# Optimization experiments

Hardware: AMD Instinct MI355X
Metric: run time of the kernel (lower is better)

## Reference

```python
import jax, jax.numpy as jnp
import numpy as np

B, T, C = 8, 2048, 1024
H = 4 * C
N_LAYER, LAYER_ID = 12, 2
K_CLAMP = 60.0
LN_EPS = 1e-5


def _ln(x, g, b):
    m = jnp.mean(x, axis=-1, keepdims=True)
    v = jnp.var(x, axis=-1, keepdims=True)
    return (x - m) * jax.lax.rsqrt(v + LN_EPS) * g + b


def _mix(x, time_mix, combined_mix):
    # x: (B,T,C). Causal shift (zeros at t=0), anti-causal shift (zeros at t=T-1).
    c = x.shape[-1]
    xm1 = jnp.pad(x[:, :-1], ((0, 0), (1, 0), (0, 0)))
    xp1 = jnp.pad(x[:, 1:], ((0, 0), (0, 1), (0, 0)))
    xc = jnp.concatenate([xm1[..., :c // 2], xp1[..., c // 2:]], axis=-1)
    return x * time_mix + xm1 * (1.0 - time_mix) + xc * combined_mix


def _wkv(time_decay, time_first, k, v):
    # RWKV WKV exponential-decay linear recurrence (the custom CUDA kernel).
    # k, v: (B,T,C); k > 0 (already clamped+exp'd).
    # y_t = (a_t + exp(u)*k_t*v_t) / (b_t + exp(u)*k_t)
    # a_{t+1} = exp(-exp(w))*a_t + k_t*v_t ; b likewise with v=1.
    ed = jnp.exp(-jnp.exp(time_decay))  # per-step channel decay, (C,)
    eu = jnp.exp(time_first)            # current-token bonus, (C,)

    def step(carry, kv_t):
        a, b = carry
        kt, vt = kv_t
        y = (a + eu * kt * vt) / (b + eu * kt)
        return (ed * a + kt * vt, ed * b + kt), y

    kT = jnp.swapaxes(k, 0, 1)  # (T,B,C)
    vT = jnp.swapaxes(v, 0, 1)
    z = jnp.zeros_like(kT[0])
    _, y = jax.lax.scan(step, (z, z), (kT, vT))
    return jnp.swapaxes(y, 0, 1)  # (B,T,C)


def _time_mix_block(x, time_mix, combined_mix, time_decay, time_first, Wk, Wv, Wr, Wo):
    xm = _mix(x, time_mix, combined_mix)
    k = jnp.exp(jnp.minimum(xm @ Wk.T, K_CLAMP))
    v = xm @ Wv.T
    r = xm @ Wr.T
    wkv = _wkv(time_decay, time_first, k, v)
    return (jax.nn.sigmoid(r) * wkv) @ Wo.T


def _channel_mix_block(x, time_mix, combined_mix, Fk, Fv, Fr):
    xm = _mix(x, time_mix, combined_mix)
    k = jnp.square(jax.nn.relu(xm @ Fk.T))
    kv = k @ Fv.T
    return jax.nn.sigmoid(xm @ Fr.T) * kv


def setup_inputs():
    key = jax.random.key(0)
    ks = jax.random.split(key, 9)
    s = 0.02
    x = jax.random.normal(ks[0], (B, T, C), jnp.float32)
    # time_decay init per the module (f1/f2 interpolation over layers)
    h = np.arange(C, dtype=np.float64)
    frac = (LAYER_ID - 1) / (N_LAYER - 2)
    f1 = 3.0 + frac * (1.2 - 3.0)
    f2 = 0.65 + frac * (0.4 - 0.65)
    decay_speed = np.power(f2, h / (C - 1) * 7.0) * f1
    tm = jnp.concatenate([jnp.zeros(C // 2), jnp.ones(C // 2)]).reshape(1, 1, C).astype(jnp.float32)
    return dict(
        x=x,
        ln1_g=jnp.ones((C,), jnp.float32), ln1_b=jnp.zeros((C,), jnp.float32),
        ln2_g=jnp.ones((C,), jnp.float32), ln2_b=jnp.zeros((C,), jnp.float32),
        att_time_mix=tm,
        att_combined_mix=jnp.full((1, 1, C), 0.01, jnp.float32),
        time_decay=jnp.asarray(np.log(decay_speed), jnp.float32),
        time_first=jnp.full((C,), float(np.log(0.3)), jnp.float32),
        Wk=jax.random.normal(ks[1], (C, C), jnp.float32) * s,
        Wv=jax.random.normal(ks[2], (C, C), jnp.float32) * s,
        Wr=jax.random.normal(ks[3], (C, C), jnp.float32) * s,
        Wo=jax.random.normal(ks[4], (C, C), jnp.float32) * s,
        ffn_time_mix=tm,
        ffn_combined_mix=jnp.full((1, 1, C), 0.01, jnp.float32),
        Fk=jax.random.normal(ks[5], (H, C), jnp.float32) * s,
        Fv=jax.random.normal(ks[6], (C, H), jnp.float32) * s,
        Fr=jax.random.normal(ks[7], (C, C), jnp.float32) * s,
    )


def reference(x, ln1_g, ln1_b, ln2_g, ln2_b, att_time_mix, att_combined_mix,
              time_decay, time_first, Wk, Wv, Wr, Wo,
              ffn_time_mix, ffn_combined_mix, Fk, Fv, Fr):
    x = _ln(x, ln1_g, ln1_b)
    x = x + _time_mix_block(x, att_time_mix, att_combined_mix, time_decay, time_first, Wk, Wv, Wr, Wo)
    x = _ln(x, ln2_g, ln2_b)
    x = x + _channel_mix_block(x, ffn_time_mix, ffn_combined_mix, Fk, Fv, Fr)
    return x
```

## Files before the change

### kernel.cpp

```cpp
#include <hip/hip_runtime.h>
#include <hip/hip_bf16.h>

typedef float f32x4 __attribute__((ext_vector_type(4)));
typedef __bf16 bf16x8 __attribute__((ext_vector_type(8)));
typedef __bf16 bf16x4 __attribute__((ext_vector_type(4)));

#define DEVI static __device__ __forceinline__

DEVI void glds16(const void* g, void* l) {
  __builtin_amdgcn_global_load_lds((__attribute__((address_space(1))) void*)g,
                                   (__attribute__((address_space(3))) void*)l, 16, 0, 0);
}

DEVI f32x4 load4(const float* p) { return *(const f32x4*)p; }
DEVI f32x4 load4(const __bf16* p) {
  bf16x4 v = *(const bf16x4*)p;
  f32x4 o = { (float)v[0], (float)v[1], (float)v[2], (float)v[3] };
  return o;
}
DEVI void store4(float* p, f32x4 v) { *(f32x4*)p = v; }
DEVI void store4(__bf16* p, f32x4 v) {
  bf16x4 o = { (__bf16)v[0], (__bf16)v[1], (__bf16)v[2], (__bf16)v[3] };
  *(bf16x4*)p = o;
}

__global__ void cvt_bf16(const float* __restrict__ in, __bf16* __restrict__ out, int n4) {
  int i = blockIdx.x * 256 + threadIdx.x;
  if (i < n4) {
    f32x4 v = *(const f32x4*)(in + (size_t)i * 4);
    store4(out + (size_t)i * 4, v);
  }
}

template <typename TIN, typename TOUT>
__global__ __launch_bounds__(256) void ln_kernel(const TIN* __restrict__ x,
    const float* __restrict__ gw, const float* __restrict__ bw,
    TOUT* __restrict__ out) {
  const size_t row = blockIdx.x;
  f32x4 v = load4(x + row * 1024 + threadIdx.x * 4);
  float s = v[0] + v[1] + v[2] + v[3];
  float q = v[0]*v[0] + v[1]*v[1] + v[2]*v[2] + v[3]*v[3];
#pragma unroll
  for (int o = 32; o > 0; o >>= 1) { s += __shfl_down(s, o); q += __shfl_down(q, o); }
  __shared__ float ss[4], qq[4];
  const int w = threadIdx.x >> 6, l = threadIdx.x & 63;
  if (l == 0) { ss[w] = s; qq[w] = q; }
  __syncthreads();
  s = ss[0] + ss[1] + ss[2] + ss[3];
  q = qq[0] + qq[1] + qq[2] + qq[3];
  const float mean = s * (1.0f / 1024.0f);
  const float var = q * (1.0f / 1024.0f) - mean * mean;
  const float rstd = rsqrtf(var + 1e-5f);
  f32x4 g4 = *(const f32x4*)(gw + threadIdx.x * 4);
  f32x4 b4 = *(const f32x4*)(bw + threadIdx.x * 4);
  f32x4 o;
#pragma unroll
  for (int j = 0; j < 4; ++j) o[j] = (v[j] - mean) * rstd * g4[j] + b4[j];
  store4(out + row * 1024 + threadIdx.x * 4, o);
}

template <typename TIN>
__global__ __launch_bounds__(256) void mix_kernel(const TIN* __restrict__ x,
    const float* __restrict__ tm, const float* __restrict__ cm,
    __bf16* __restrict__ out) {
  const int idx = blockIdx.x * 256 + threadIdx.x;
  const int t = (idx >> 8) & 2047;
  const int c = (idx & 255) * 4;
  const size_t base = ((size_t)(idx >> 8) << 10) + c;
  f32x4 xv = load4(x + base);
  f32x4 xm1 = {0.f, 0.f, 0.f, 0.f}, xp1 = {0.f, 0.f, 0.f, 0.f};
  if (t > 0)    xm1 = load4(x + base - 1024);
  if (t < 2047) xp1 = load4(x + base + 1024);
  f32x4 tm4 = *(const f32x4*)(tm + c);
  f32x4 cm4 = *(const f32x4*)(cm + c);
  f32x4 xc = (c < 512) ? xm1 : xp1;
  f32x4 o;
#pragma unroll
  for (int j = 0; j < 4; ++j)
    o[j] = xv[j] * tm4[j] + xm1[j] * (1.0f - tm4[j]) + xc[j] * cm4[j];
  store4(out + base, o);
}

__global__ __launch_bounds__(256) void wkv_part(const __bf16* __restrict__ k,
    const __bf16* __restrict__ v, const float* __restrict__ td,
    float* __restrict__ scA, float* __restrict__ scB) {
  const int gid = blockIdx.x * 256 + threadIdx.x;
  const int c = gid & 1023;
  const int j = (gid >> 10) & 31;
  const int b = gid >> 15;
  const float ed = expf(-expf(td[c]));
  float A = 0.f, Bv = 0.f;
  size_t off = ((size_t)(b * 2048 + j * 64) << 10) + c;
#pragma unroll 4
  for (int i = 0; i < 64; ++i, off += 1024) {
    const float kt = (float)k[off];
    const float kv = kt * (float)v[off];
    A = ed * A + kv;
    Bv = ed * Bv + kt;
  }
  scA[gid] = A;
  scB[gid] = Bv;
}

__global__ __launch_bounds__(256) void wkv_scan(const float* __restrict__ td,
    float* __restrict__ scA, float* __restrict__ scB) {
  const int gid = blockIdx.x * 256 + threadIdx.x;
  const int c = gid & 1023;
  const int b = gid >> 10;
  const float edL = expf(-expf(td[c]) * 64.0f);
  float a = 0.f, bb = 0.f;
  size_t off = ((size_t)b << 15) + c;
  for (int j = 0; j < 32; ++j, off += 1024) {
    const float Aj = scA[off], Bj = scB[off];
    scA[off] = a;
    scB[off] = bb;
    a = edL * a + Aj;
    bb = edL * bb + Bj;
  }
}

__global__ __launch_bounds__(256) void wkv_apply(const __bf16* __restrict__ k,
    const __bf16* __restrict__ v, const __bf16* __restrict__ sr,
    const float* __restrict__ td, const float* __restrict__ tf,
    const float* __restrict__ scA, const float* __restrict__ scB,
    __bf16* __restrict__ srw) {
  const int gid = blockIdx.x * 256 + threadIdx.x;
  const int c = gid & 1023;
  const int j = (gid >> 10) & 31;
  const int b = gid >> 15;
  const float ed = expf(-expf(td[c]));
  const float eu = expf(tf[c]);
  float a = scA[gid], bb = scB[gid];
  size_t off = ((size_t)(b * 2048 + j * 64) << 10) + c;
#pragma unroll 4
  for (int i = 0; i < 64; ++i, off += 1024) {
    const float kt = (float)k[off];
    const float vt = (float)v[off];
    const float kv = kt * vt;
    const float y = (a + eu * kv) / (bb + eu * kt);
    srw[off] = (__bf16)((float)sr[off] * y);
    a = ed * a + kv;
    bb = ed * bb + kt;
  }
}

enum { EPI_NONE = 0, EPI_EXP, EPI_SIG, EPI_RELU2, EPI_RESID, EPI_FINAL, EPI_KVR };

#define SCHED0() __builtin_amdgcn_sched_barrier(0)
#define SBAR() { __builtin_amdgcn_s_barrier(); SCHED0(); }
#define VMW0() { asm volatile("s_waitcnt vmcnt(0)" ::: "memory"); SCHED0(); }
#define LGKM(n) { asm volatile("s_waitcnt lgkmcnt(" #n ")" ::: "memory"); SCHED0(); }

template <int EPI>
__global__ __launch_bounds__(256, 2) void gemm128(
    const __bf16* __restrict__ A, const __bf16* __restrict__ W,
    void* outp, const void* res, const void* sig, const int N, const int K) {
  __shared__ __bf16 sA[2][8192];
  __shared__ __bf16 sB[2][8192];
  const int tid = threadIdx.x;
  const int w = tid >> 6, l = tid & 63;
  const int wr = (w >> 1) << 6, wc = (w & 1) << 6;

  const int nwg = gridDim.x * gridDim.y;
  int wg = blockIdx.y * gridDim.x + blockIdx.x;
  wg = (wg & 7) * (nwg >> 3) + (wg >> 3);
  const int m0 = (wg / gridDim.x) << 7;
  const int n0 = (wg % gridDim.x) << 7;

  const int lr = l >> 3;
  const int lc = (l & 7) ^ lr;
  const size_t gA = (size_t)(m0 + w * 32 + lr) * K + lc * 8;
  const size_t gB = (size_t)(n0 + w * 32 + lr) * K + lc * 8;
  const int ldsD = w * 2048;

  const int NTK = K >> 6;

#define STG_A(buf, kt, g) glds16(A + gA + (size_t)(g) * 8 * K + (size_t)(kt) * 64, &sA[buf][ldsD + (g) * 512])
#define STG_B(buf, kt, g) glds16(W + gB + (size_t)(g) * 8 * K + (size_t)(kt) * 64, &sB[buf][ldsD + (g) * 512])

  const int rA = (wr + (l & 15)) * 64;
  const int rB = (wc + (l & 15)) * 64;
  const int csw = l & 7;
  const int k0 = l >> 4;
#define LDA(buf, mi, kk) (*(const bf16x8*)&sA[buf][rA + (mi) * 1024 + ((((kk) * 4 + k0) ^ csw) << 3)])
#define LDB(buf, ni, kk) (*(const bf16x8*)&sB[buf][rB + (ni) * 1024 + ((((kk) * 4 + k0) ^ csw) << 3)])

  f32x4 acc[4][4] = {};

#pragma unroll
  for (int g = 0; g < 4; ++g) STG_A(0, 0, g);
#pragma unroll
  for (int g = 0; g < 4; ++g) STG_B(0, 0, g);

  for (int kt = 0; kt < NTK; ++kt) {
    const int buf = kt & 1, nb = buf ^ 1;
    const bool st = (kt + 1 < NTK);
    VMW0();
    SBAR();
    if (st) {
#pragma unroll
      for (int g = 0; g < 4; ++g) STG_A(nb, kt + 1, g);
#pragma unroll
      for (int g = 0; g < 4; ++g) STG_B(nb, kt + 1, g);
    }
    SCHED0();
    bf16x8 a0[4], a1[4], b0[4], b1[4];
#pragma unroll
    for (int i = 0; i < 4; ++i) a0[i] = LDA(buf, i, 0);
#pragma unroll
    for (int i = 0; i < 4; ++i) b0[i] = LDB(buf, i, 0);
    SCHED0();
#pragma unroll
    for (int i = 0; i < 4; ++i) a1[i] = LDA(buf, i, 1);
#pragma unroll
    for (int i = 0; i < 4; ++i) b1[i] = LDB(buf, i, 1);
    SCHED0();
    LGKM(8);
    __builtin_amdgcn_s_setprio(1);
#pragma unroll
    for (int mi = 0; mi < 4; ++mi)
#pragma unroll
      for (int ni = 0; ni < 4; ++ni)
        acc[mi][ni] = __builtin_amdgcn_mfma_f32_16x16x32_bf16(a0[mi], b0[ni], acc[mi][ni], 0, 0, 0);
    __builtin_amdgcn_s_setprio(0); SCHED0();
    LGKM(0);
    __builtin_amdgcn_s_setprio(1);
#pragma unroll
    for (int mi = 0; mi < 4; ++mi)
#pragma unroll
      for (int ni = 0; ni < 4; ++ni)
        acc[mi][ni] = __builtin_amdgcn_mfma_f32_16x16x32_bf16(a1[mi], b1[ni], acc[mi][ni], 0, 0, 0);
    __builtin_amdgcn_s_setprio(0);
  }

  const int rl = (l >> 4) << 2, cl = l & 15;
#pragma unroll
  for (int mi = 0; mi < 4; ++mi) {
#pragma unroll
    for (int ni = 0; ni < 4; ++ni) {
#pragma unroll
      for (int e = 0; e < 4; ++e) {
        const int r = m0 + wr + mi * 16 + rl + e;
        const int cidx = n0 + wc + ni * 16 + cl;
        const size_t idx = (size_t)r * N + cidx;
        const float vacc = acc[mi][ni][e];
        if constexpr (EPI == EPI_NONE) {
          ((__bf16*)outp)[idx] = (__bf16)vacc;
        } else if constexpr (EPI == EPI_EXP) {
          ((__bf16*)outp)[idx] = (__bf16)expf(fminf(vacc, 60.0f));
        } else if constexpr (EPI == EPI_SIG) {
          ((__bf16*)outp)[idx] = (__bf16)(1.0f / (1.0f + expf(-vacc)));
        } else if constexpr (EPI == EPI_RELU2) {
          const float rv = fmaxf(vacc, 0.0f);
          ((__bf16*)outp)[idx] = (__bf16)(rv * rv);
        } else if constexpr (EPI == EPI_RESID) {
          ((__bf16*)outp)[idx] = (__bf16)(vacc + (float)((const __bf16*)res)[idx]);
        } else if constexpr (EPI == EPI_FINAL) {
          ((float*)outp)[idx] = ((const float*)res)[idx] + (float)((const __bf16*)sig)[idx] * vacc;
        } else {
          const int sel = cidx >> 10;
          const size_t oidx = (size_t)r * 1024 + (cidx & 1023);
          if (sel == 0)      ((__bf16*)outp)[oidx] = (__bf16)expf(fminf(vacc, 60.0f));
          else if (sel == 1) ((__bf16*)const_cast<void*>(res))[oidx] = (__bf16)vacc;
          else               ((__bf16*)const_cast<void*>(sig))[oidx] = (__bf16)(1.0f / (1.0f + expf(-vacc)));
        }
      }
    }
  }
}

extern "C" void kernel_launch(void* const* d_in, const int* in_sizes, int n_in,
                              void* d_out, int out_size, void* d_ws, size_t ws_size,
                              hipStream_t stream) {
  (void)in_sizes; (void)n_in; (void)out_size;
  const float* x    = (const float*)d_in[0];
  const float* ln1g = (const float*)d_in[1];
  const float* ln1b = (const float*)d_in[2];
  const float* ln2g = (const float*)d_in[3];
  const float* ln2b = (const float*)d_in[4];
  const float* atm  = (const float*)d_in[5];
  const float* acm  = (const float*)d_in[6];
  const float* td   = (const float*)d_in[7];
  const float* tf   = (const float*)d_in[8];
  const float* Wk   = (const float*)d_in[9];
  const float* Wv   = (const float*)d_in[10];
  const float* Wr   = (const float*)d_in[11];
  const float* Wo   = (const float*)d_in[12];
  const float* ftm  = (const float*)d_in[13];
  const float* fcm  = (const float*)d_in[14];
  const float* Fk   = (const float*)d_in[15];
  const float* Fv   = (const float*)d_in[16];
  const float* Fr   = (const float*)d_in[17];

  constexpr size_t C = 1024, T = 2048, Bs = 8, H = 4096;
  constexpr size_t NT = Bs * T;
  constexpr size_t NTC = NT * C;
  constexpr size_t CC = C * C;
  constexpr size_t CH = C * H;

  char* p = (char*)d_ws;
  auto takeb = [&](size_t elems) { __bf16* q = (__bf16*)p; p += elems * 2; return q; };
  __bf16* wKVR = takeb(3 * CC);
  __bf16* wWo  = takeb(CC);
  __bf16* wFk  = takeb(CH);
  __bf16* wFv  = takeb(CH);
  __bf16* wFr  = takeb(CC);
  __bf16* Ab   = takeb(NTC);
  __bf16* Bb   = takeb(NTC);
  __bf16* Db   = takeb(NTC);
  float* scA = (float*)p; p += Bs * 32 * C * 4;
  float* scB = (float*)p; p += Bs * 32 * C * 4;
  __bf16* kk = (__bf16*)p;
  const size_t used = (size_t)(p - (char*)d_ws);
  const size_t kkcap = ws_size > used ? ws_size - used : 0;
  int chunks = 4;
  if (kkcap >= NT * H * 2)          chunks = 1;
  else if (kkcap >= NT * H)         chunks = 2;
  __bf16* Cb = kk;
  __bf16* sr  = (__bf16*)d_out;
  float*  x3  = (float*)d_out;

  auto cvt = [&](const float* src, size_t n, __bf16* dst) {
    const int n4 = (int)(n / 4);
    cvt_bf16<<<dim3((n4 + 255) / 256), dim3(256), 0, stream>>>(src, dst, n4);
  };
  cvt(Wk, CC, wKVR); cvt(Wv, CC, wKVR + CC); cvt(Wr, CC, wKVR + 2 * CC);
  cvt(Wo, CC, wWo); cvt(Fk, CH, wFk); cvt(Fv, CH, wFv); cvt(Fr, CC, wFr);

  const dim3 blk(256);

  ln_kernel<float, __bf16><<<dim3((unsigned)NT), blk, 0, stream>>>(x, ln1g, ln1b, Ab);
  mix_kernel<__bf16><<<dim3((unsigned)(NTC / 1024)), blk, 0, stream>>>(Ab, atm, acm, Bb);
  gemm128<EPI_KVR><<<dim3(24, 128), blk, 0, stream>>>(Bb, wKVR, Cb, Db, sr, 3072, 1024);
  wkv_part<<<dim3(1024), blk, 0, stream>>>(Cb, Db, td, scA, scB);
  wkv_scan<<<dim3(32), blk, 0, stream>>>(td, scA, scB);
  wkv_apply<<<dim3(1024), blk, 0, stream>>>(Cb, Db, sr, td, tf, scA, scB, Bb);
  gemm128<EPI_RESID><<<dim3(8, 128), blk, 0, stream>>>(Bb, wWo, Ab, Ab, nullptr, 1024, 1024);
  ln_kernel<__bf16, float><<<dim3((unsigned)NT), blk, 0, stream>>>(Ab, ln2g, ln2b, x3);
  mix_kernel<float><<<dim3((unsigned)(NTC / 1024)), blk, 0, stream>>>(x3, ftm, fcm, Db);
  gemm128<EPI_SIG><<<dim3(8, 128), blk, 0, stream>>>(Db, wFr, Bb, nullptr, nullptr, 1024, 1024);
  const size_t Mc = NT / chunks;
  for (int ch = 0; ch < chunks; ++ch) {
    const size_t ro = (size_t)ch * Mc;
    gemm128<EPI_RELU2><<<dim3(32, (unsigned)(Mc / 128)), blk, 0, stream>>>(
        Db + ro * C, wFk, kk, nullptr, nullptr, 4096, 1024);
    gemm128<EPI_FINAL><<<dim3(8, (unsigned)(Mc / 128)), blk, 0, stream>>>(
        kk, wFv, (float*)d_out + ro * C, (const float*)d_out + ro * C,
        Bb + ro * C, 1024, 4096);
  }
}
```

Measured before the change: 798.3 us.

## Vectorize WKV kernels, merge weight conversion, simplify GEMM to single-buffered LDS

The three WKV kernels now handle four channels per thread with vector bf16/f32 loads and use a quarter of the blocks. The seven weight-conversion launches become one kernel writing into a contiguous workspace. The GEMM drops LDS double buffering, the explicit waitcnt/sched barriers, setprio and the occupancy hint, and uses plain __syncthreads around each K-tile load. That GEMM change removes the overlap of global-to-LDS copies with MFMA work, so the dominant GEMMs are likely to lose throughput, while the WKV and launch changes save only a little.

```diff
diff --git a/kernel.cpp b/kernel.cpp
--- a/kernel.cpp
+++ b/kernel.cpp
@@ -24,12 +24,28 @@
   *(bf16x4*)p = o;
 }
 
-__global__ void cvt_bf16(const float* __restrict__ in, __bf16* __restrict__ out, int n4) {
-  int i = blockIdx.x * 256 + threadIdx.x;
-  if (i < n4) {
-    f32x4 v = *(const f32x4*)(in + (size_t)i * 4);
-    store4(out + (size_t)i * 4, v);
-  }
+constexpr size_t C = 1024, T = 2048, Bs = 8, H = 4096;
+constexpr size_t NT = Bs * T;
+constexpr size_t NTC = NT * C;
+constexpr size_t CC = C * C;
+constexpr size_t CH = C * H;
+
+__global__ __launch_bounds__(256) void cvt_all(
+    const float* __restrict__ Wk, const float* __restrict__ Wv,
+    const float* __restrict__ Wr, const float* __restrict__ Wo,
+    const float* __restrict__ Fk, const float* __restrict__ Fv,
+    const float* __restrict__ Fr, __bf16* __restrict__ out) {
+  const size_t e = ((size_t)blockIdx.x * 256 + threadIdx.x) * 4;
+  const float* src; size_t rel;
+  if      (e < CC)          { src = Wk; rel = e; }
+  else if (e < 2 * CC)      { src = Wv; rel = e - CC; }
+  else if (e < 3 * CC)      { src = Wr; rel = e - 2 * CC; }
+  else if (e < 4 * CC)      { src = Wo; rel = e - 3 * CC; }
+  else if (e < 4 * CC + CH) { src = Fk; rel = e - 4 * CC; }
+  else if (e < 4 * CC + 2 * CH) { src = Fv; rel = e - 4 * CC - CH; }
+  else                      { src = Fr; rel = e - 4 * CC - 2 * CH; }
+  f32x4 v = *(const f32x4*)(src + rel);
+  store4(out + e, v);
 }
 
 template <typename TIN, typename TOUT>
@@ -85,37 +101,51 @@
     const __bf16* __restrict__ v, const float* __restrict__ td,
     float* __restrict__ scA, float* __restrict__ scB) {
   const int gid = blockIdx.x * 256 + threadIdx.x;
-  const int c = gid & 1023;
-  const int j = (gid >> 10) & 31;
-  const int b = gid >> 15;
-  const float ed = expf(-expf(td[c]));
-  float A = 0.f, Bv = 0.f;
+  const int c = (gid & 255) * 4;
+  const int j = (gid >> 8) & 31;
+  const int b = gid >> 13;
+  float ed[4], A[4] = {}, Bv[4] = {};
+#pragma unroll
+  for (int q = 0; q < 4; ++q) ed[q] = expf(-expf(td[c + q]));
   size_t off = ((size_t)(b * 2048 + j * 64) << 10) + c;
-#pragma unroll 4
   for (int i = 0; i < 64; ++i, off += 1024) {
-    const float kt = (float)k[off];
-    const float kv = kt * (float)v[off];
-    A = ed * A + kv;
-    Bv = ed * Bv + kt;
-  }
-  scA[gid] = A;
-  scB[gid] = Bv;
+    bf16x4 k4 = *(const bf16x4*)(k + off);
+    bf16x4 v4 = *(const bf16x4*)(v + off);
+#pragma unroll
+    for (int q = 0; q < 4; ++q) {
+      const float kt = (float)k4[q];
+      A[q] = ed[q] * A[q] + kt * (float)v4[q];
+      Bv[q] = ed[q] * Bv[q] + kt;
+    }
+  }
+  const size_t sidx = (((size_t)b * 32 + j) << 10) + c;
+  f32x4 oA = { A[0], A[1], A[2], A[3] };
+  f32x4 oB = { Bv[0], Bv[1], Bv[2], Bv[3] };
+  *(f32x4*)(scA + sidx) = oA;
+  *(f32x4*)(scB + sidx) = oB;
 }
 
 __global__ __launch_bounds__(256) void wkv_scan(const float* __restrict__ td,
     float* __restrict__ scA, float* __restrict__ scB) {
   const int gid = blockIdx.x * 256 + threadIdx.x;
-  const int c = gid & 1023;
-  const int b = gid >> 10;
-  const float edL = expf(-expf(td[c]) * 64.0f);
-  float a = 0.f, bb = 0.f;
+  const int c = (gid & 255) * 4;
+  const int b = gid >> 8;
+  float edL[4], a[4] = {}, bb[4] = {};
+#pragma unroll
+  for (int q = 0; q < 4; ++q) edL[q] = expf(-expf(td[c + q]) * 64.0f);
   size_t off = ((size_t)b << 15) + c;
   for (int j = 0; j < 32; ++j, off += 1024) {
-    const float Aj = scA[off], Bj = scB[off];
-    scA[off] = a;
-    scB[off] = bb;
-    a = edL * a + Aj;
-    bb = edL * bb + Bj;
+    f32x4 Aj = *(const f32x4*)(scA + off);
+    f32x4 Bj = *(const f32x4*)(scB + off);
+    f32x4 ca = { a[0], a[1], a[2], a[3] };
+    f32x4 cb = { bb[0], bb[1], bb[2], bb[3] };
+    *(f32x4*)(scA + off) = ca;
+    *(f32x4*)(scB + off) = cb;
+#pragma unroll
+    for (int q = 0; q < 4; ++q) {
+      a[q] = edL[q] * a[q] + Aj[q];
+      bb[q] = edL[q] * bb[q] + Bj[q];
+    }
   }
 }
 
@@ -125,38 +155,44 @@
     const float* __restrict__ scA, const float* __restrict__ scB,
     __bf16* __restrict__ srw) {
   const int gid = blockIdx.x * 256 + threadIdx.x;
-  const int c = gid & 1023;
-  const int j = (gid >> 10) & 31;
-  const int b = gid >> 15;
-  const float ed = expf(-expf(td[c]));
-  const float eu = expf(tf[c]);
-  float a = scA[gid], bb = scB[gid];
+  const int c = (gid & 255) * 4;
+  const int j = (gid >> 8) & 31;
+  const int b = gid >> 13;
+  float ed[4], eu[4], a[4], bb[4];
+#pragma unroll
+  for (int q = 0; q < 4; ++q) { ed[q] = expf(-expf(td[c + q])); eu[q] = expf(tf[c + q]); }
+  const size_t sidx = (((size_t)b * 32 + j) << 10) + c;
+  f32x4 ca = *(const f32x4*)(scA + sidx);
+  f32x4 cb = *(const f32x4*)(scB + sidx);
+#pragma unroll
+  for (int q = 0; q < 4; ++q) { a[q] = ca[q]; bb[q] = cb[q]; }
   size_t off = ((size_t)(b * 2048 + j * 64) << 10) + c;
-#pragma unroll 4
   for (int i = 0; i < 64; ++i, off += 1024) {
-    const float kt = (float)k[off];
-    const float vt = (float)v[off];
-    const float kv = kt * vt;
-    const float y = (a + eu * kv) / (bb + eu * kt);
-    srw[off] = (__bf16)((float)sr[off] * y);
-    a = ed * a + kv;
-    bb = ed * bb + kt;
+    bf16x4 k4 = *(const bf16x4*)(k + off);
+    bf16x4 v4 = *(const bf16x4*)(v + off);
+    bf16x4 s4 = *(const bf16x4*)(sr + off);
+    bf16x4 o4;
+#pragma unroll
+    for (int q = 0; q < 4; ++q) {
+      const float kt = (float)k4[q];
+      const float kv = kt * (float)v4[q];
+      const float y = (a[q] + eu[q] * kv) / (bb[q] + eu[q] * kt);
+      o4[q] = (__bf16)((float)s4[q] * y);
+      a[q] = ed[q] * a[q] + kv;
+      bb[q] = ed[q] * bb[q] + kt;
+    }
+    *(bf16x4*)(srw + off) = o4;
   }
 }
 
 enum { EPI_NONE = 0, EPI_EXP, EPI_SIG, EPI_RELU2, EPI_RESID, EPI_FINAL, EPI_KVR };
 
-#define SCHED0() __builtin_amdgcn_sched_barrier(0)
-#define SBAR() { __builtin_amdgcn_s_barrier(); SCHED0(); }
-#define VMW0() { asm volatile("s_waitcnt vmcnt(0)" ::: "memory"); SCHED0(); }
-#define LGKM(n) { asm volatile("s_waitcnt lgkmcnt(" #n ")" ::: "memory"); SCHED0(); }
-
 template <int EPI>
-__global__ __launch_bounds__(256, 2) void gemm128(
+__global__ __launch_bounds__(256) void gemm128(
     const __bf16* __restrict__ A, const __bf16* __restrict__ W,
     void* outp, const void* res, const void* sig, const int N, const int K) {
-  __shared__ __bf16 sA[2][8192];
-  __shared__ __bf16 sB[2][8192];
+  __shared__ __bf16 sA[8192];
+  __shared__ __bf16 sB[8192];
   const int tid = threadIdx.x;
   const int w = tid >> 6, l = tid & 63;
   const int wr = (w >> 1) << 6, wc = (w & 1) << 6;
@@ -175,62 +211,44 @@
 
   const int NTK = K >> 6;
 
-#define STG_A(buf, kt, g) glds16(A + gA + (size_t)(g) * 8 * K + (size_t)(kt) * 64, &sA[buf][ldsD + (g) * 512])
-#define STG_B(buf, kt, g) glds16(W + gB + (size_t)(g) * 8 * K + (size_t)(kt) * 64, &sB[buf][ldsD + (g) * 512])
+#define STG_A(kt, g) glds16(A + gA + (size_t)(g) * 8 * K + (size_t)(kt) * 64, &sA[ldsD + (g) * 512])
+#define STG_B(kt, g) glds16(W + gB + (size_t)(g) * 8 * K + (size_t)(kt) * 64, &sB[ldsD + (g) * 512])
 
   const int rA = (wr + (l & 15)) * 64;
   const int rB = (wc + (l & 15)) * 64;
   const int csw = l & 7;
   const int k0 = l >> 4;
-#define LDA(buf, mi, kk) (*(const bf16x8*)&sA[buf][rA + (mi) * 1024 + ((((kk) * 4 + k0) ^ csw) << 3)])
-#define LDB(buf, ni, kk) (*(const bf16x8*)&sB[buf][rB + (ni) * 1024 + ((((kk) * 4 + k0) ^ csw) << 3)])
+#define LDA(mi, kk) (*(const bf16x8*)&sA[rA + (mi) * 1024 + ((((kk) * 4 + k0) ^ csw) << 3)])
+#define LDB(ni, kk) (*(const bf16x8*)&sB[rB + (ni) * 1024 + ((((kk) * 4 + k0) ^ csw) << 3)])
 
   f32x4 acc[4][4] = {};
 
-#pragma unroll
-  for (int g = 0; g < 4; ++g) STG_A(0, 0, g);
-#pragma unroll
-  for (int g = 0; g < 4; ++g) STG_B(0, 0, g);
-
   for (int kt = 0; kt < NTK; ++kt) {
-    const int buf = kt & 1, nb = buf ^ 1;
-    const bool st = (kt + 1 < NTK);
-    VMW0();
-    SBAR();
-    if (st) {
-#pragma unroll
-      for (int g = 0; g < 4; ++g) STG_A(nb, kt + 1, g);
-#pragma unroll
-      for (int g = 0; g < 4; ++g) STG_B(nb, kt + 1, g);
-    }
-    SCHED0();
+    if (kt) __syncthreads();
+#pragma unroll
+    for (int g = 0; g < 4; ++g) STG_A(kt, g);
+#pragma unroll
+    for (int g = 0; g < 4; ++g) STG_B(kt, g);
+    __syncthreads();
     bf16x8 a0[4], a1[4], b0[4], b1[4];
 #pragma unroll
-    for (int i = 0; i < 4; ++i) a0[i] = LDA(buf, i, 0);
-#pragma unroll
-    for (int i = 0; i < 4; ++i) b0[i] = LDB(buf, i, 0);
-    SCHED0();
-#pragma unroll
-    for (int i = 0; i < 4; ++i) a1[i] = LDA(buf, i, 1);
-#pragma unroll
-    for (int i = 0; i < 4; ++i) b1[i] = LDB(buf, i, 1);
-    SCHED0();
-    LGKM(8);
-    __builtin_amdgcn_s_setprio(1);
+    for (int i = 0; i < 4; ++i) a0[i] = LDA(i, 0);
+#pragma unroll
+    for (int i = 0; i < 4; ++i) b0[i] = LDB(i, 0);
+#pragma unroll
+    for (int i = 0; i < 4; ++i) a1[i] = LDA(i, 1);
+#pragma unroll
+    for (int i = 0; i < 4; ++i) b1[i] = LDB(i, 1);
 #pragma unroll
     for (int mi = 0; mi < 4; ++mi)
 #pragma unroll
       for (int ni = 0; ni < 4; ++ni)
         acc[mi][ni] = __builtin_amdgcn_mfma_f32_16x16x32_bf16(a0[mi], b0[ni], acc[mi][ni], 0, 0, 0);
-    __builtin_amdgcn_s_setprio(0); SCHED0();
-    LGKM(0);
-    __builtin_amdgcn_s_setprio(1);
 #pragma unroll
     for (int mi = 0; mi < 4; ++mi)
 #pragma unroll
       for (int ni = 0; ni < 4; ++ni)
         acc[mi][ni] = __builtin_amdgcn_mfma_f32_16x16x32_bf16(a1[mi], b1[ni], acc[mi][ni], 0, 0, 0);
-    __builtin_amdgcn_s_setprio(0);
   }
 
   const int rl = (l >> 4) << 2, cl = l & 15;
@@ -292,12 +310,6 @@
   const float* Fv   = (const float*)d_in[16];
   const float* Fr   = (const float*)d_in[17];
 
-  constexpr size_t C = 1024, T = 2048, Bs = 8, H = 4096;
-  constexpr size_t NT = Bs * T;
-  constexpr size_t NTC = NT * C;
-  constexpr size_t CC = C * C;
-  constexpr size_t CH = C * H;
-
   char* p = (char*)d_ws;
   auto takeb = [&](size_t elems) { __bf16* q = (__bf16*)p; p += elems * 2; return q; };
   __bf16* wKVR = takeb(3 * CC);
@@ -320,21 +332,17 @@
   __bf16* sr  = (__bf16*)d_out;
   float*  x3  = (float*)d_out;
 
-  auto cvt = [&](const float* src, size_t n, __bf16* dst) {
-    const int n4 = (int)(n / 4);
-    cvt_bf16<<<dim3((n4 + 255) / 256), dim3(256), 0, stream>>>(src, dst, n4);
-  };
-  cvt(Wk, CC, wKVR); cvt(Wv, CC, wKVR + CC); cvt(Wr, CC, wKVR + 2 * CC);
-  cvt(Wo, CC, wWo); cvt(Fk, CH, wFk); cvt(Fv, CH, wFv); cvt(Fr, CC, wFr);
-
   const dim3 blk(256);
+
+  cvt_all<<<dim3((unsigned)((5 * CC + 2 * CH) / 4 / 256)), blk, 0, stream>>>(
+      Wk, Wv, Wr, Wo, Fk, Fv, Fr, wKVR);
 
   ln_kernel<float, __bf16><<<dim3((unsigned)NT), blk, 0, stream>>>(x, ln1g, ln1b, Ab);
   mix_kernel<__bf16><<<dim3((unsigned)(NTC / 1024)), blk, 0, stream>>>(Ab, atm, acm, Bb);
   gemm128<EPI_KVR><<<dim3(24, 128), blk, 0, stream>>>(Bb, wKVR, Cb, Db, sr, 3072, 1024);
-  wkv_part<<<dim3(1024), blk, 0, stream>>>(Cb, Db, td, scA, scB);
-  wkv_scan<<<dim3(32), blk, 0, stream>>>(td, scA, scB);
-  wkv_apply<<<dim3(1024), blk, 0, stream>>>(Cb, Db, sr, td, tf, scA, scB, Bb);
+  wkv_part<<<dim3(256), blk, 0, stream>>>(Cb, Db, td, scA, scB);
+  wkv_scan<<<dim3(8), blk, 0, stream>>>(td, scA, scB);
+  wkv_apply<<<dim3(256), blk, 0, stream>>>(Cb, Db, sr, td, tf, scA, scB, Bb);
   gemm128<EPI_RESID><<<dim3(8, 128), blk, 0, stream>>>(Bb, wWo, Ab, Ab, nullptr, 1024, 1024);
   ln_kernel<__bf16, float><<<dim3((unsigned)NT), blk, 0, stream>>>(Ab, ln2g, ln2b, x3);
   mix_kernel<float><<<dim3((unsigned)(NTC / 1024)), blk, 0, stream>>>(x3, ftm, fcm, Db);
```

Result: no change. 786.3 us (-1.5%).
